# Kernel tuning notes

Hardware: AMD Instinct MI355X
Metric: run time of the kernel (lower is better)

The kernel has to match this reference:

```python
import jax, jax.numpy as jnp
import numpy as np


def setup_inputs() -> dict:
    key = jax.random.key(0)
    ks = jax.random.split(key, 5)
    B, NINS, NHID = 128, 4096, 128
    inputs = jax.random.normal(ks[0], (B, NINS, NHID), dtype=jnp.float32)
    claims = jax.random.normal(ks[1], (B, NHID), dtype=jnp.float32)  # unused by forward
    # project: Linear(2*nhid -> 64) -> ReLU -> Linear(64 -> 1)
    W1 = jax.random.normal(ks[2], (2 * NHID, 64), dtype=jnp.float32) * (1.0 / np.sqrt(2 * NHID))
    b1 = jnp.zeros((64,), dtype=jnp.float32)
    W2 = jax.random.normal(ks[3], (64, 1), dtype=jnp.float32) * (1.0 / np.sqrt(64))
    b2 = jnp.zeros((1,), dtype=jnp.float32)
    return {"inputs": inputs, "index": 5, "claims": claims,
            "W1": W1, "b1": b1, "W2": W2, "b2": b2}


def reference(inputs, index, claims, W1, b1, W2, b2):
    # inputs: [B, nins, nhid]
    B, NINS, NHID = inputs.shape
    own = jax.lax.dynamic_slice_in_dim(inputs, index, 1, axis=1)  # [B, 1, nhid]
    own = jnp.broadcast_to(own, (B, NINS, NHID))                  # repeat over nins
    tmp = jnp.concatenate([own, inputs], axis=2)                  # [B, nins, 2*nhid]
    h = jax.nn.relu(jnp.einsum('bnd,dk->bnk', tmp, W1) + b1)      # [B, nins, 64]
    att = jnp.einsum('bnk,ko->bno', h, W2) + b2                   # [B, nins, 1]
    weights = jax.nn.softmax(att[..., 0], axis=1)                 # [B, nins]
    outputs = jnp.einsum('bnd,bn->bd', inputs, weights)           # [B, nhid]
    return outputs
```

## Files before the change

### kernel.cpp

```cpp
#include <hip/hip_runtime.h>
#include <math.h>

#define BATCH 128
#define NINS  4096
#define NHID  128
#define KH    64
#define NPART 128
#define PART_STRIDE 136
#define O_OFF 8
#define TPW 2
#define XP 136

typedef __attribute__((ext_vector_type(8))) short short8;
typedef __attribute__((ext_vector_type(4))) float f32x4;

__device__ inline unsigned short f2bf(float f) {
    union { float f; unsigned u; } v; v.f = f;
    return (unsigned short)((v.u + 0x7FFFu + ((v.u >> 16) & 1u)) >> 16);
}

__device__ inline unsigned cvt_pk_u32(float a, float b) {
#if __has_builtin(__builtin_amdgcn_cvt_pk_bf16_f32)
    typedef __attribute__((ext_vector_type(2))) __bf16 bf16x2;
    bf16x2 p = __builtin_amdgcn_cvt_pk_bf16_f32(a, b);
    unsigned u; __builtin_memcpy(&u, &p, 4); return u;
#else
    return (unsigned)f2bf(a) | ((unsigned)f2bf(b) << 16);
#endif
}

__global__ void precompute_c(const float* __restrict__ inputs,
                             const int* __restrict__ index_p,
                             const float* __restrict__ W1,
                             const float* __restrict__ b1,
                             float* __restrict__ c) {
    const int b = blockIdx.x;
    const int k = threadIdx.x;
    const int idx = index_p[0];
    const float* own = inputs + ((size_t)b * NINS + idx) * NHID;
    float acc = b1[k];
    #pragma unroll 8
    for (int d = 0; d < NHID; ++d)
        acc = fmaf(own[d], W1[d * KH + k], acc);
    c[b * KH + k] = acc;
}

__global__ __launch_bounds__(256, 3)
void att_partial(const float* __restrict__ inputs,
                 const float* __restrict__ W1,
                 const float* __restrict__ W2,
                 const float* __restrict__ b2_p,
                 const float* __restrict__ c,
                 float* __restrict__ part) {
    __shared__ unsigned short WbT[KH][XP];
    __shared__ unsigned short Xs[4][32][XP];
    __shared__ float ebuf[4][32];

    const int tid  = threadIdx.x;
    const int lane = tid & 63;
    const int wv   = tid >> 6;
    const int b    = blockIdx.y;
    const int quad = lane >> 4;
    const int m16  = lane & 15;

    const float* xb = inputs + (size_t)b * NINS * NHID;

    {
        const int n  = tid >> 2;
        const int kb = (tid & 3) * 32;
        const float* wp = W1 + (size_t)(NHID + kb) * KH + n;
        #pragma unroll
        for (int j = 0; j < 32; j += 2) {
            unsigned u = cvt_pk_u32(wp[(size_t)j * KH], wp[(size_t)(j + 1) * KH]);
            *(unsigned*)&WbT[n][kb + j] = u;
        }
    }
    __syncthreads();

    float w2v[4];
    #pragma unroll
    for (int nf = 0; nf < 4; ++nf) w2v[nf] = W2[nf * 16 + m16];
    const float b2v = b2_p[0];
    float cv[4];
    #pragma unroll
    for (int nf = 0; nf < 4; ++nf) cv[nf] = c[b * KH + nf * 16 + m16];

    const int base = (blockIdx.x * 4 + wv) * TPW;

    auto stage = [&](int n0) {
        const float* src = xb + (size_t)n0 * NHID;
        unsigned short* xw = &Xs[wv][0][0];
        #pragma unroll
        for (int i = 0; i < 16; ++i) {
            const int f = i * 64 + lane;
            f32x4 v = *(const f32x4*)(src + (size_t)f * 4);
            uint2 u;
            u.x = cvt_pk_u32(v.x, v.y);
            u.y = cvt_pk_u32(v.z, v.w);
            *(uint2*)(xw + (f >> 5) * XP + (f & 31) * 4) = u;
        }
    };

    stage(base * 32);

    for (int t = 0; t < TPW; ++t) {
        const int tile = base + t;
        const int n0   = tile * 32;

        short8 Af[2][4];
        #pragma unroll
        for (int mf = 0; mf < 2; ++mf)
            #pragma unroll
            for (int ks = 0; ks < 4; ++ks)
                Af[mf][ks] = *(const short8*)&Xs[wv][mf * 16 + m16][ks * 32 + quad * 8];

        if (t + 1 < TPW) stage((tile + 1) * 32);

        f32x4 acc[2][4];
        #pragma unroll
        for (int mf = 0; mf < 2; ++mf)
            #pragma unroll
            for (int nf = 0; nf < 4; ++nf) {
                f32x4 z = {cv[nf], cv[nf], cv[nf], cv[nf]};
                acc[mf][nf] = z;
            }

        #pragma unroll
        for (int ks = 0; ks < 4; ++ks) {
            short8 Bf[4];
            #pragma unroll
            for (int nf = 0; nf < 4; ++nf)
                Bf[nf] = *(const short8*)&WbT[nf * 16 + m16][ks * 32 + quad * 8];
            #pragma unroll
            for (int mf = 0; mf < 2; ++mf)
                #pragma unroll
                for (int nf = 0; nf < 4; ++nf)
                    acc[mf][nf] = __builtin_amdgcn_mfma_f32_16x16x32_bf16(
                        Af[mf][ks], Bf[nf], acc[mf][nf], 0, 0, 0);
        }

        float att[2][4];
        #pragma unroll
        for (int mf = 0; mf < 2; ++mf)
            #pragma unroll
            for (int r = 0; r < 4; ++r) {
                float s = 0.0f;
                #pragma unroll
                for (int nf = 0; nf < 4; ++nf)
                    s = fmaf(fmaxf(acc[mf][nf][r], 0.0f), w2v[nf], s);
                s += __shfl_xor(s, 1);
                s += __shfl_xor(s, 2);
                s += __shfl_xor(s, 4);
                s += __shfl_xor(s, 8);
                att[mf][r] = s + b2v;
            }

        float mx = att[0][0];
        #pragma unroll
        for (int mf = 0; mf < 2; ++mf)
            #pragma unroll
            for (int r = 0; r < 4; ++r) mx = fmaxf(mx, att[mf][r]);
        mx = fmaxf(mx, __shfl_xor(mx, 16));
        mx = fmaxf(mx, __shfl_xor(mx, 32));

        float ev[2][4];
        float L = 0.0f;
        #pragma unroll
        for (int mf = 0; mf < 2; ++mf)
            #pragma unroll
            for (int r = 0; r < 4; ++r) {
                ev[mf][r] = __expf(att[mf][r] - mx);
                L += ev[mf][r];
            }
        L += __shfl_xor(L, 16);
        L += __shfl_xor(L, 32);

        if (m16 == 0) {
            #pragma unroll
            for (int mf = 0; mf < 2; ++mf)
                #pragma unroll
                for (int r = 0; r < 4; ++r)
                    ebuf[wv][mf * 16 + quad * 4 + r] = ev[mf][r];
        }

        const int G  = lane >> 5;
        const int db = (lane & 31) * 4;
        f32x4 e4[4];
        #pragma unroll
        for (int i = 0; i < 4; ++i)
            e4[i] = *(const f32x4*)&ebuf[wv][G * 16 + i * 4];

        f32x4 o = {0.0f, 0.0f, 0.0f, 0.0f};
        const float* xr = xb + (size_t)(n0 + G * 16) * NHID + db;
        #pragma unroll
        for (int jj = 0; jj < 16; ++jj) {
            f32x4 xv = *(const f32x4*)(xr + (size_t)jj * NHID);
            o += xv * e4[jj >> 2][jj & 3];
        }
        #pragma unroll
        for (int i = 0; i < 4; ++i) o[i] += __shfl_xor(o[i], 32);

        float* p = part + (size_t)(b * NPART + tile) * PART_STRIDE;
        if (lane == 0) { p[0] = mx; p[1] = L; }
        if (lane < 32) *(f32x4*)(p + O_OFF + db) = o;
    }
}

__global__ void finalize(const float* __restrict__ part,
                         float* __restrict__ out) {
    const int b = blockIdx.x;
    const int d = threadIdx.x;
    const float* pb = part + (size_t)b * NPART * PART_STRIDE;

    float M = pb[0];
    #pragma unroll 8
    for (int p = 1; p < NPART; ++p)
        M = fmaxf(M, pb[p * PART_STRIDE]);

    float S = 0.0f, acc = 0.0f;
    #pragma unroll 4
    for (int p = 0; p < NPART; ++p) {
        const float sc = __expf(pb[p * PART_STRIDE] - M);
        S   = fmaf(sc, pb[p * PART_STRIDE + 1], S);
        acc = fmaf(sc, pb[p * PART_STRIDE + O_OFF + d], acc);
    }
    out[b * NHID + d] = acc / S;
}

extern "C" void kernel_launch(void* const* d_in, const int* in_sizes, int n_in,
                              void* d_out, int out_size, void* d_ws, size_t ws_size,
                              hipStream_t stream) {
    const float* inputs = (const float*)d_in[0];
    const int*   index  = (const int*)  d_in[1];
    const float* W1     = (const float*)d_in[3];
    const float* b1     = (const float*)d_in[4];
    const float* W2     = (const float*)d_in[5];
    const float* b2     = (const float*)d_in[6];
    float* out = (float*)d_out;

    float* c    = (float*)d_ws;
    float* part = c + BATCH * KH;

    precompute_c<<<dim3(BATCH), dim3(64), 0, stream>>>(inputs, index, W1, b1, c);

    dim3 gB(NPART / (4 * TPW), BATCH);
    att_partial<<<gB, dim3(256), 0, stream>>>(inputs, W1, W2, b2, c, part);

    finalize<<<dim3(BATCH), dim3(NHID), 0, stream>>>(part, out);
}
```

Measured before the change: 412.9 us.

## Load MFMA A fragments directly from global, drop LDS staging, parallelize finalize

The attention kernel no longer stages each 32-row input tile into shared memory. Each lane now loads its own bf16 MFMA A-fragment straight from global memory and converts it in registers. With the large LDS buffer gone, the occupancy hint rises from 3 to 4 blocks. The finalize kernel now spreads the max and sum over partials across threads with shuffle reductions and precomputes the scale factors in shared memory instead of running two serial loops per thread. The risk is that the direct global loads are strided per row, losing the coalesced staging and the overlap of the next tile's load.

```diff
diff --git a/kernel.cpp b/kernel.cpp
--- a/kernel.cpp
+++ b/kernel.cpp
@@ -13,6 +13,7 @@
 
 typedef __attribute__((ext_vector_type(8))) short short8;
 typedef __attribute__((ext_vector_type(4))) float f32x4;
+typedef __attribute__((ext_vector_type(4))) unsigned int u32x4;
 
 __device__ inline unsigned short f2bf(float f) {
     union { float f; unsigned u; } v; v.f = f;
@@ -45,7 +46,7 @@
     c[b * KH + k] = acc;
 }
 
-__global__ __launch_bounds__(256, 3)
+__global__ __launch_bounds__(256, 4)
 void att_partial(const float* __restrict__ inputs,
                  const float* __restrict__ W1,
                  const float* __restrict__ W2,
@@ -53,7 +54,6 @@
                  const float* __restrict__ c,
                  float* __restrict__ part) {
     __shared__ unsigned short WbT[KH][XP];
-    __shared__ unsigned short Xs[4][32][XP];
     __shared__ float ebuf[4][32];
 
     const int tid  = threadIdx.x;
@@ -87,34 +87,27 @@
 
     const int base = (blockIdx.x * 4 + wv) * TPW;
 
-    auto stage = [&](int n0) {
-        const float* src = xb + (size_t)n0 * NHID;
-        unsigned short* xw = &Xs[wv][0][0];
-        #pragma unroll
-        for (int i = 0; i < 16; ++i) {
-            const int f = i * 64 + lane;
-            f32x4 v = *(const f32x4*)(src + (size_t)f * 4);
-            uint2 u;
-            u.x = cvt_pk_u32(v.x, v.y);
-            u.y = cvt_pk_u32(v.z, v.w);
-            *(uint2*)(xw + (f >> 5) * XP + (f & 31) * 4) = u;
-        }
-    };
-
-    stage(base * 32);
-
+    #pragma unroll
     for (int t = 0; t < TPW; ++t) {
         const int tile = base + t;
         const int n0   = tile * 32;
 
         short8 Af[2][4];
         #pragma unroll
-        for (int mf = 0; mf < 2; ++mf)
-            #pragma unroll
-            for (int ks = 0; ks < 4; ++ks)
-                Af[mf][ks] = *(const short8*)&Xs[wv][mf * 16 + m16][ks * 32 + quad * 8];
-
-        if (t + 1 < TPW) stage((tile + 1) * 32);
+        for (int mf = 0; mf < 2; ++mf) {
+            const float* rp = xb + (size_t)(n0 + mf * 16 + m16) * NHID + quad * 8;
+            #pragma unroll
+            for (int ks = 0; ks < 4; ++ks) {
+                f32x4 v0 = *(const f32x4*)(rp + ks * 32);
+                f32x4 v1 = *(const f32x4*)(rp + ks * 32 + 4);
+                u32x4 u;
+                u.x = cvt_pk_u32(v0.x, v0.y);
+                u.y = cvt_pk_u32(v0.z, v0.w);
+                u.z = cvt_pk_u32(v1.x, v1.y);
+                u.w = cvt_pk_u32(v1.z, v1.w);
+                __builtin_memcpy(&Af[mf][ks], &u, 16);
+            }
+        }
 
         f32x4 acc[2][4];
         #pragma unroll
@@ -208,22 +201,45 @@
 
 __global__ void finalize(const float* __restrict__ part,
                          float* __restrict__ out) {
+    __shared__ float esc[NPART];
+    __shared__ float wred[2][2];
+
     const int b = blockIdx.x;
     const int d = threadIdx.x;
+    const int w = d >> 6;
     const float* pb = part + (size_t)b * NPART * PART_STRIDE;
 
-    float M = pb[0];
+    const float m = pb[(size_t)d * PART_STRIDE];
+    const float l = pb[(size_t)d * PART_STRIDE + 1];
+
+    float mm = m;
+    mm = fmaxf(mm, __shfl_xor(mm, 1));
+    mm = fmaxf(mm, __shfl_xor(mm, 2));
+    mm = fmaxf(mm, __shfl_xor(mm, 4));
+    mm = fmaxf(mm, __shfl_xor(mm, 8));
+    mm = fmaxf(mm, __shfl_xor(mm, 16));
+    mm = fmaxf(mm, __shfl_xor(mm, 32));
+    if ((d & 63) == 0) wred[0][w] = mm;
+    __syncthreads();
+    const float M = fmaxf(wred[0][0], wred[0][1]);
+
+    const float e = __expf(m - M);
+    esc[d] = e;
+    float s = e * l;
+    s += __shfl_xor(s, 1);
+    s += __shfl_xor(s, 2);
+    s += __shfl_xor(s, 4);
+    s += __shfl_xor(s, 8);
+    s += __shfl_xor(s, 16);
+    s += __shfl_xor(s, 32);
+    if ((d & 63) == 0) wred[1][w] = s;
+    __syncthreads();
+    const float S = wred[1][0] + wred[1][1];
+
+    float acc = 0.0f;
     #pragma unroll 8
-    for (int p = 1; p < NPART; ++p)
-        M = fmaxf(M, pb[p * PART_STRIDE]);
-
-    float S = 0.0f, acc = 0.0f;
-    #pragma unroll 4
-    for (int p = 0; p < NPART; ++p) {
-        const float sc = __expf(pb[p * PART_STRIDE] - M);
-        S   = fmaf(sc, pb[p * PART_STRIDE + 1], S);
-        acc = fmaf(sc, pb[p * PART_STRIDE + O_OFF + d], acc);
-    }
+    for (int p = 0; p < NPART; ++p)
+        acc = fmaf(esc[p], pb[(size_t)p * PART_STRIDE + O_OFF + d], acc);
     out[b * NHID + d] = acc / S;
 }
 
```

New measurement: 395.6 us. 1.04x faster.
